# Kernel tuning notes

Hardware: AMD Instinct MI355X
Metric: run time of the kernel (lower is better)

## Reference

```python
import jax, jax.numpy as jnp
import numpy as np

KH, KW = 3, 3
PAD, STRIDE = 1, 1
KD = 3  # depth kernel extent; extended with one zero slice -> 4 indices


def _unfold(x, pad, stride):
    # x: (B, C, H, W) -> (B, C, KH*KW, oH, oW), patches ordered row-major like F.unfold
    B, C, H, W = x.shape
    xp = jnp.pad(x, ((0, 0), (0, 0), (pad, pad), (pad, pad)))
    oH = (H + 2 * pad - KH) // stride + 1
    oW = (W + 2 * pad - KW) // stride + 1
    pats = [xp[:, :, i:i + (oH - 1) * stride + 1:stride, j:j + (oW - 1) * stride + 1:stride]
            for i in range(KH) for j in range(KW)]
    return jnp.stack(pats, axis=2)


def setup_inputs() -> dict:
    key = jax.random.key(0)
    k1, k2, k3 = jax.random.split(key, 3)
    features = jax.random.normal(k1, (4, 16, 512, 512), dtype=jnp.float32)
    depth = jax.random.randint(k2, (4, 512, 512), 0, 8, dtype=jnp.int32)
    weight = jax.random.normal(k3, (32, 16, 3, 3, 3), dtype=jnp.float32) * 0.05
    return {"features": features, "depth": depth, "weight": weight}


def reference(features, depth, weight):
    oC, iC = weight.shape[0], weight.shape[1]
    # unfolded input patches: (B, iC, 9, oH, oW)
    patches = _unfold(features, PAD, STRIDE)
    # unfolded depth: (B, 9, oH, oW); padding fills with depth 0 (matches F.unfold)
    dpat = _unfold(depth[:, None, :, :].astype(jnp.int32), PAD, STRIDE)[:, 0]
    center = dpat[:, KH * KW // 2][:, None]  # (B, 1, oH, oW)
    diff = dpat - center
    # diff < -1 or diff >= 1 -> select appended zero slice (index 3); else diff+1
    idx = jnp.where((diff < -1) | (diff >= 1), 3, diff + 1)  # (B, 9, oH, oW) in [0, 3]
    onehot = jax.nn.one_hot(idx, KD + 1, dtype=features.dtype)  # (B, 9, oH, oW, 4)
    # extended weight with zero depth-slice: (oC, iC, 4, 9)
    ext_w = jnp.concatenate([weight, jnp.zeros_like(weight[:, :, :1])], axis=2)
    ext_w = ext_w.reshape(oC, iC, KD + 1, KH * KW)
    # per-pixel depth-gated 3x3x3 conv (bias is never added in the original op)
    out = jnp.einsum('oidk,bkhwd,bikhw->bohw', ext_w, onehot, patches)
    return out
```

## Files before the change

kernel.cpp:

```cpp
#include <hip/hip_runtime.h>


#define IC 16
#define OC 32
#define Hh 512
#define Ww 512
#define HW (Hh * Ww)

typedef __attribute__((ext_vector_type(8))) short short8;
typedef __attribute__((ext_vector_type(4))) float float4v;
typedef __attribute__((ext_vector_type(2))) unsigned int uint2v;
typedef __attribute__((ext_vector_type(4))) unsigned int uint4v;

__device__ __forceinline__ unsigned short f2bf(float x) {
    unsigned u = __float_as_uint(x);
    unsigned r = u + 0x7FFFu + ((u >> 16) & 1u);
    return (unsigned short)(r >> 16);
}

__global__ void prep_weights(const float* __restrict__ wgt,
                             unsigned short* __restrict__ wsA) {
    int e = blockIdx.x * 256 + threadIdx.x;
    if (e >= 9 * 2 * 64 * 8) return;
    int j    = e & 7;
    int lane = (e >> 3) & 63;
    int mt   = (e >> 9) & 1;
    int c    = e >> 10;
    int oc = mt * 16 + (lane & 15);
    int kk = ((lane >> 4) << 3) + j;
    wsA[e] = f2bf(wgt[oc * 432 + (kk >> 1) * 27 + (kk & 1) * 9 + c]);
}

__global__ __launch_bounds__(256) void prep_feat(const float* __restrict__ feat,
                                                 unsigned short* __restrict__ ft) {
    int p = blockIdx.x * 256 + threadIdx.x;
    int b = p >> 18, hw = p & (HW - 1);
    const float* fp = feat + (size_t)b * IC * HW + hw;
    unsigned pk[8];
#pragma unroll
    for (int i = 0; i < 8; ++i) {
        float a = fp[(size_t)(2 * i) * HW];
        float c = fp[(size_t)(2 * i + 1) * HW];
        pk[i] = (unsigned)f2bf(a) | ((unsigned)f2bf(c) << 16);
    }
    uint4v* dst = (uint4v*)(ft + (size_t)p * 16);
    dst[0] = (uint4v){pk[0], pk[1], pk[2], pk[3]};
    dst[1] = (uint4v){pk[4], pk[5], pk[6], pk[7]};
}

__global__ __launch_bounds__(256) void depconv_mfma_t(
    const unsigned short* __restrict__ ft,
    const int*   __restrict__ depth,
    const unsigned short* __restrict__ wsA,
    float*       __restrict__ out)
{
    const int tid  = threadIdx.x;
    const int lane = tid & 63;
    const int wv   = tid >> 6;
    const int g    = lane >> 4;
    const int n    = lane & 15;

    short8 afrag[9][2];
    {
        const short8* ap = (const short8*)wsA;
#pragma unroll
        for (int c = 0; c < 9; ++c) {
            afrag[c][0] = ap[(c * 2 + 0) * 64 + lane];
            afrag[c][1] = ap[(c * 2 + 1) * 64 + lane];
        }
    }

    const int P0    = blockIdx.x * 256;
    const int b     = P0 >> 18;
    const int hw0   = P0 & (HW - 1);
    const int h     = hw0 >> 9;
    const int wbase = (hw0 & (Ww - 1)) + wv * 64;

    const int y0 = (h == 0) ? 0 : h - 1;
    const int y2 = (h == Hh - 1) ? Hh - 1 : h + 1;
    const unsigned short* frow[3];
    const int* drow[3];
    frow[0] = ft + ((size_t)((b << 18) + y0 * Ww) << 4);
    frow[1] = ft + ((size_t)((b << 18) + h  * Ww) << 4);
    frow[2] = ft + ((size_t)((b << 18) + y2 * Ww) << 4);
    drow[0] = depth + (b << 18) + y0 * Ww;
    drow[1] = depth + (b << 18) + h  * Ww;
    drow[2] = depth + (b << 18) + y2 * Ww;

    for (int it = 0; it < 4; ++it) {
        const int w  = wbase + it * 16 + n;
        const int dc = drow[1][w];
        const int x0 = (w == 0) ? 0 : w - 1;
        const int x2 = (w == Ww - 1) ? Ww - 1 : w + 1;
        const int xs[3] = {x0, w, x2};

        float4v acc0 = {0.f, 0.f, 0.f, 0.f};
        float4v acc1 = {0.f, 0.f, 0.f, 0.f};

#pragma unroll
        for (int t = 0; t < 9; ++t) {
            const int kh = t / 3, kw = t % 3;
            unsigned mm;
            if (t == 4) {
                mm = 0xffff0000u;
            } else {
                const bool inb = !((kh == 0 && h == 0) || (kh == 2 && h == Hh - 1) ||
                                   (kw == 0 && w == 0) || (kw == 2 && w == Ww - 1));
                const int dn   = drow[kh][xs[kw]];
                const int diff = dn - dc;
                mm = (diff == 0) ? 0xffff0000u : ((diff == -1) ? 0x0000ffffu : 0u);
                if (!inb) mm = 0u;
            }
            const uint2v pr = *(const uint2v*)(frow[kh] + (((size_t)xs[kw]) << 4) + g * 4);
            union { short8 s; unsigned u[4]; } bf;
            bf.u[0] = __builtin_amdgcn_perm(0u, pr.x, 0x01000100u) & mm;
            bf.u[1] = __builtin_amdgcn_perm(0u, pr.x, 0x03020302u) & mm;
            bf.u[2] = __builtin_amdgcn_perm(0u, pr.y, 0x01000100u) & mm;
            bf.u[3] = __builtin_amdgcn_perm(0u, pr.y, 0x03020302u) & mm;

            acc0 = __builtin_amdgcn_mfma_f32_16x16x32_bf16(afrag[t][0], bf.s, acc0, 0, 0, 0);
            acc1 = __builtin_amdgcn_mfma_f32_16x16x32_bf16(afrag[t][1], bf.s, acc1, 0, 0, 0);
        }

        const int rbase = g * 4;
        float* op = out + ((size_t)(b * OC) << 18) + h * Ww + w;
#pragma unroll
        for (int r = 0; r < 4; ++r) {
            op[(size_t)(rbase + r) * HW]      = acc0[r];
            op[(size_t)(16 + rbase + r) * HW] = acc1[r];
        }
    }
}

__global__ __launch_bounds__(256) void depconv_mfma_reg(
    const float* __restrict__ feat,
    const int*   __restrict__ depth,
    const unsigned short* __restrict__ wsA,
    float*       __restrict__ out)
{
    const int tid  = threadIdx.x;
    const int lane = tid & 63;
    const int wv   = tid >> 6;
    const int g    = lane >> 4;
    const int n    = lane & 15;

    short8 afrag[9][2];
    {
        const short8* ap = (const short8*)wsA;
#pragma unroll
        for (int c = 0; c < 9; ++c) {
            afrag[c][0] = ap[(c * 2 + 0) * 64 + lane];
            afrag[c][1] = ap[(c * 2 + 1) * 64 + lane];
        }
    }

    const int P0    = blockIdx.x * 256;
    const int b     = P0 >> 18;
    const int hw0   = P0 & (HW - 1);
    const int h     = hw0 >> 9;
    const int wbase = (hw0 & (Ww - 1)) + wv * 64;
    const int* __restrict__ drow = depth + (b << 18) + h * Ww;

    for (int it = 0; it < 4; ++it) {
        const int w  = wbase + it * 16 + n;
        const int dc = drow[w];
        const float* __restrict__ fb = feat + (size_t)(b * IC + g * 4) * HW + (h - 1) * Ww + (w - 1);
        const int*   __restrict__ db = depth + (b << 18) + (h - 1) * Ww + (w - 1);

        float4v acc0 = {0.f, 0.f, 0.f, 0.f};
        float4v acc1 = {0.f, 0.f, 0.f, 0.f};
#pragma unroll
        for (int t = 0; t < 9; ++t) {
            const int kh = t / 3, kw = t % 3;
            const int y = h + kh - 1;
            const int x = w + kw - 1;
            const bool inb = ((unsigned)y < (unsigned)Hh) & ((unsigned)x < (unsigned)Ww);
            unsigned pk0 = 0, pk1 = 0, pk2 = 0, pk3 = 0;
            if (inb) {
                const int dn   = db[kh * Ww + kw];
                const int diff = dn - dc;
                const bool m0 = (diff == -1);
                const bool m1 = (diff == 0);
                const unsigned short u0 = f2bf(fb[0 * HW + kh * Ww + kw]);
                const unsigned short u1 = f2bf(fb[1 * HW + kh * Ww + kw]);
                const unsigned short u2 = f2bf(fb[2 * HW + kh * Ww + kw]);
                const unsigned short u3 = f2bf(fb[3 * HW + kh * Ww + kw]);
                pk0 = (m0 ? (unsigned)u0 : 0u) | ((m1 ? (unsigned)u0 : 0u) << 16);
                pk1 = (m0 ? (unsigned)u1 : 0u) | ((m1 ? (unsigned)u1 : 0u) << 16);
                pk2 = (m0 ? (unsigned)u2 : 0u) | ((m1 ? (unsigned)u2 : 0u) << 16);
                pk3 = (m0 ? (unsigned)u3 : 0u) | ((m1 ? (unsigned)u3 : 0u) << 16);
            }
            union { short8 s; unsigned u[4]; } bfv;
            bfv.u[0] = pk0; bfv.u[1] = pk1; bfv.u[2] = pk2; bfv.u[3] = pk3;
            acc0 = __builtin_amdgcn_mfma_f32_16x16x32_bf16(afrag[t][0], bfv.s, acc0, 0, 0, 0);
            acc1 = __builtin_amdgcn_mfma_f32_16x16x32_bf16(afrag[t][1], bfv.s, acc1, 0, 0, 0);
        }

        const int rbase = g * 4;
        float* op = out + ((size_t)(b * OC) << 18) + h * Ww + w;
#pragma unroll
        for (int r = 0; r < 4; ++r) {
            op[(size_t)(rbase + r) * HW]      = acc0[r];
            op[(size_t)(16 + rbase + r) * HW] = acc1[r];
        }
    }
}

extern "C" void kernel_launch(void* const* d_in, const int* in_sizes, int n_in,
                              void* d_out, int out_size, void* d_ws, size_t ws_size,
                              hipStream_t stream) {
    const float* feat  = (const float*)d_in[0];
    const int*   depth = (const int*)d_in[1];
    const float* wgt   = (const float*)d_in[2];
    float* out = (float*)d_out;

    unsigned short* wsA = (unsigned short*)d_ws;
    unsigned short* ft  = (unsigned short*)((char*)d_ws + 32768);

    prep_weights<<<36, 256, 0, stream>>>(wgt, wsA);

    const int total = 4 * HW;
    if (ws_size >= (size_t)32768 + (size_t)total * IC * 2) {
        prep_feat<<<total / 256, 256, 0, stream>>>(feat, ft);
        depconv_mfma_t<<<total / 256, 256, 0, stream>>>(ft, depth, wsA, out);
    } else {
        depconv_mfma_reg<<<total / 256, 256, 0, stream>>>(feat, depth, wsA, out);
    }
}
```

Measured before the change: 247.4 us.

## Fuse feature bf16 prep into conv kernel via shared-memory row tiles

```diff
diff --git a/kernel.cpp b/kernel.cpp
--- a/kernel.cpp
+++ b/kernel.cpp
@@ -10,7 +10,6 @@
 typedef __attribute__((ext_vector_type(8))) short short8;
 typedef __attribute__((ext_vector_type(4))) float float4v;
 typedef __attribute__((ext_vector_type(2))) unsigned int uint2v;
-typedef __attribute__((ext_vector_type(4))) unsigned int uint4v;
 
 __device__ __forceinline__ unsigned short f2bf(float x) {
     unsigned u = __float_as_uint(x);
@@ -31,34 +30,60 @@
     wsA[e] = f2bf(wgt[oc * 432 + (kk >> 1) * 27 + (kk & 1) * 9 + c]);
 }
 
-__global__ __launch_bounds__(256) void prep_feat(const float* __restrict__ feat,
-                                                 unsigned short* __restrict__ ft) {
-    int p = blockIdx.x * 256 + threadIdx.x;
-    int b = p >> 18, hw = p & (HW - 1);
-    const float* fp = feat + (size_t)b * IC * HW + hw;
-    unsigned pk[8];
-#pragma unroll
-    for (int i = 0; i < 8; ++i) {
-        float a = fp[(size_t)(2 * i) * HW];
-        float c = fp[(size_t)(2 * i + 1) * HW];
-        pk[i] = (unsigned)f2bf(a) | ((unsigned)f2bf(c) << 16);
-    }
-    uint4v* dst = (uint4v*)(ft + (size_t)p * 16);
-    dst[0] = (uint4v){pk[0], pk[1], pk[2], pk[3]};
-    dst[1] = (uint4v){pk[4], pk[5], pk[6], pk[7]};
-}
-
-__global__ __launch_bounds__(256) void depconv_mfma_t(
-    const unsigned short* __restrict__ ft,
+__global__ __launch_bounds__(256) void depconv_fused(
+    const float* __restrict__ feat,
     const int*   __restrict__ depth,
     const unsigned short* __restrict__ wsA,
     float*       __restrict__ out)
 {
+    __shared__ unsigned short ftile[3][258][IC];
+    __shared__ int            dtile[3][258];
+
     const int tid  = threadIdx.x;
     const int lane = tid & 63;
     const int wv   = tid >> 6;
     const int g    = lane >> 4;
     const int n    = lane & 15;
+
+    const int bid = blockIdx.x;
+    const int wg  = (bid & 7) * (4096 / 8) + (bid >> 3);
+
+    const int P0     = wg * 256;
+    const int b      = P0 >> 18;
+    const int hw0    = P0 & (HW - 1);
+    const int h      = hw0 >> 9;
+    const int wstart = hw0 & (Ww - 1);
+
+    const int y0 = (h == 0) ? 0 : h - 1;
+    const int y2 = (h == Hh - 1) ? Hh - 1 : h + 1;
+    const int yrs[3] = {y0, h, y2};
+
+    {
+        const int x  = wstart - 1 + tid;
+        const int xc = x < 0 ? 0 : (x > Ww - 1 ? Ww - 1 : x);
+        const int xt = wstart - 1 + 256 + tid;
+        const int xct = xt > Ww - 1 ? Ww - 1 : xt;
+#pragma unroll
+        for (int r = 0; r < 3; ++r) {
+            const float* fpl = feat + (size_t)b * IC * HW + (size_t)yrs[r] * Ww;
+            const int*   dpl = depth + (b << 18) + yrs[r] * Ww;
+            dtile[r][tid] = dpl[xc];
+            if (tid < 2) dtile[r][256 + tid] = dpl[xct];
+#pragma unroll
+            for (int icp = 0; icp < 8; ++icp) {
+                float a = fpl[(size_t)(2 * icp) * HW + xc];
+                float c = fpl[(size_t)(2 * icp + 1) * HW + xc];
+                *(unsigned*)&ftile[r][tid][2 * icp] =
+                    (unsigned)f2bf(a) | ((unsigned)f2bf(c) << 16);
+                if (tid < 2) {
+                    float at = fpl[(size_t)(2 * icp) * HW + xct];
+                    float ct = fpl[(size_t)(2 * icp + 1) * HW + xct];
+                    *(unsigned*)&ftile[r][256 + tid][2 * icp] =
+                        (unsigned)f2bf(at) | ((unsigned)f2bf(ct) << 16);
+                }
+            }
+        }
+    }
 
     short8 afrag[9][2];
     {
@@ -69,30 +94,12 @@
             afrag[c][1] = ap[(c * 2 + 1) * 64 + lane];
         }
     }
-
-    const int P0    = blockIdx.x * 256;
-    const int b     = P0 >> 18;
-    const int hw0   = P0 & (HW - 1);
-    const int h     = hw0 >> 9;
-    const int wbase = (hw0 & (Ww - 1)) + wv * 64;
-
-    const int y0 = (h == 0) ? 0 : h - 1;
-    const int y2 = (h == Hh - 1) ? Hh - 1 : h + 1;
-    const unsigned short* frow[3];
-    const int* drow[3];
-    frow[0] = ft + ((size_t)((b << 18) + y0 * Ww) << 4);
-    frow[1] = ft + ((size_t)((b << 18) + h  * Ww) << 4);
-    frow[2] = ft + ((size_t)((b << 18) + y2 * Ww) << 4);
-    drow[0] = depth + (b << 18) + y0 * Ww;
-    drow[1] = depth + (b << 18) + h  * Ww;
-    drow[2] = depth + (b << 18) + y2 * Ww;
+    __syncthreads();
 
     for (int it = 0; it < 4; ++it) {
-        const int w  = wbase + it * 16 + n;
-        const int dc = drow[1][w];
-        const int x0 = (w == 0) ? 0 : w - 1;
-        const int x2 = (w == Ww - 1) ? Ww - 1 : w + 1;
-        const int xs[3] = {x0, w, x2};
+        const int xb = wv * 64 + it * 16 + n;
+        const int w  = wstart + xb;
+        const int dc = dtile[1][xb + 1];
 
         float4v acc0 = {0.f, 0.f, 0.f, 0.f};
         float4v acc1 = {0.f, 0.f, 0.f, 0.f};
@@ -106,12 +113,11 @@
             } else {
                 const bool inb = !((kh == 0 && h == 0) || (kh == 2 && h == Hh - 1) ||
                                    (kw == 0 && w == 0) || (kw == 2 && w == Ww - 1));
-                const int dn   = drow[kh][xs[kw]];
-                const int diff = dn - dc;
+                const int diff = dtile[kh][xb + kw] - dc;
                 mm = (diff == 0) ? 0xffff0000u : ((diff == -1) ? 0x0000ffffu : 0u);
                 if (!inb) mm = 0u;
             }
-            const uint2v pr = *(const uint2v*)(frow[kh] + (((size_t)xs[kw]) << 4) + g * 4);
+            const uint2v pr = *(const uint2v*)(&ftile[kh][xb + kw][g << 2]);
             union { short8 s; unsigned u[4]; } bf;
             bf.u[0] = __builtin_amdgcn_perm(0u, pr.x, 0x01000100u) & mm;
             bf.u[1] = __builtin_amdgcn_perm(0u, pr.x, 0x03020302u) & mm;
@@ -120,80 +126,6 @@
 
             acc0 = __builtin_amdgcn_mfma_f32_16x16x32_bf16(afrag[t][0], bf.s, acc0, 0, 0, 0);
             acc1 = __builtin_amdgcn_mfma_f32_16x16x32_bf16(afrag[t][1], bf.s, acc1, 0, 0, 0);
-        }
-
-        const int rbase = g * 4;
-        float* op = out + ((size_t)(b * OC) << 18) + h * Ww + w;
-#pragma unroll
-        for (int r = 0; r < 4; ++r) {
-            op[(size_t)(rbase + r) * HW]      = acc0[r];
-            op[(size_t)(16 + rbase + r) * HW] = acc1[r];
-        }
-    }
-}
-
-__global__ __launch_bounds__(256) void depconv_mfma_reg(
-    const float* __restrict__ feat,
-    const int*   __restrict__ depth,
-    const unsigned short* __restrict__ wsA,
-    float*       __restrict__ out)
-{
-    const int tid  = threadIdx.x;
-    const int lane = tid & 63;
-    const int wv   = tid >> 6;
-    const int g    = lane >> 4;
-    const int n    = lane & 15;
-
-    short8 afrag[9][2];
-    {
-        const short8* ap = (const short8*)wsA;
-#pragma unroll
-        for (int c = 0; c < 9; ++c) {
-            afrag[c][0] = ap[(c * 2 + 0) * 64 + lane];
-            afrag[c][1] = ap[(c * 2 + 1) * 64 + lane];
-        }
-    }
-
-    const int P0    = blockIdx.x * 256;
-    const int b     = P0 >> 18;
-    const int hw0   = P0 & (HW - 1);
-    const int h     = hw0 >> 9;
-    const int wbase = (hw0 & (Ww - 1)) + wv * 64;
-    const int* __restrict__ drow = depth + (b << 18) + h * Ww;
-
-    for (int it = 0; it < 4; ++it) {
-        const int w  = wbase + it * 16 + n;
-        const int dc = drow[w];
-        const float* __restrict__ fb = feat + (size_t)(b * IC + g * 4) * HW + (h - 1) * Ww + (w - 1);
-        const int*   __restrict__ db = depth + (b << 18) + (h - 1) * Ww + (w - 1);
-
-        float4v acc0 = {0.f, 0.f, 0.f, 0.f};
-        float4v acc1 = {0.f, 0.f, 0.f, 0.f};
-#pragma unroll
-        for (int t = 0; t < 9; ++t) {
-            const int kh = t / 3, kw = t % 3;
-            const int y = h + kh - 1;
-            const int x = w + kw - 1;
-            const bool inb = ((unsigned)y < (unsigned)Hh) & ((unsigned)x < (unsigned)Ww);
-            unsigned pk0 = 0, pk1 = 0, pk2 = 0, pk3 = 0;
-            if (inb) {
-                const int dn   = db[kh * Ww + kw];
-                const int diff = dn - dc;
-                const bool m0 = (diff == -1);
-                const bool m1 = (diff == 0);
-                const unsigned short u0 = f2bf(fb[0 * HW + kh * Ww + kw]);
-                const unsigned short u1 = f2bf(fb[1 * HW + kh * Ww + kw]);
-                const unsigned short u2 = f2bf(fb[2 * HW + kh * Ww + kw]);
-                const unsigned short u3 = f2bf(fb[3 * HW + kh * Ww + kw]);
-                pk0 = (m0 ? (unsigned)u0 : 0u) | ((m1 ? (unsigned)u0 : 0u) << 16);
-                pk1 = (m0 ? (unsigned)u1 : 0u) | ((m1 ? (unsigned)u1 : 0u) << 16);
-                pk2 = (m0 ? (unsigned)u2 : 0u) | ((m1 ? (unsigned)u2 : 0u) << 16);
-                pk3 = (m0 ? (unsigned)u3 : 0u) | ((m1 ? (unsigned)u3 : 0u) << 16);
-            }
-            union { short8 s; unsigned u[4]; } bfv;
-            bfv.u[0] = pk0; bfv.u[1] = pk1; bfv.u[2] = pk2; bfv.u[3] = pk3;
-            acc0 = __builtin_amdgcn_mfma_f32_16x16x32_bf16(afrag[t][0], bfv.s, acc0, 0, 0, 0);
-            acc1 = __builtin_amdgcn_mfma_f32_16x16x32_bf16(afrag[t][1], bfv.s, acc1, 0, 0, 0);
         }
 
         const int rbase = g * 4;
@@ -215,15 +147,7 @@
     float* out = (float*)d_out;
 
     unsigned short* wsA = (unsigned short*)d_ws;
-    unsigned short* ft  = (unsigned short*)((char*)d_ws + 32768);
 
     prep_weights<<<36, 256, 0, stream>>>(wgt, wsA);
-
-    const int total = 4 * HW;
-    if (ws_size >= (size_t)32768 + (size_t)total * IC * 2) {
-        prep_feat<<<total / 256, 256, 0, stream>>>(feat, ft);
-        depconv_mfma_t<<<total / 256, 256, 0, stream>>>(ft, depth, wsA, out);
-    } else {
-        depconv_mfma_reg<<<total / 256, 256, 0, stream>>>(feat, depth, wsA, out);
-    }
+    depconv_fused<<<4096, 256, 0, stream>>>(feat, depth, wsA, out);
 }
```

New measurement: 265.1 us. +7.2%, slower.
